# Kernel optimization log

Hardware: AMD Instinct MI355X
Metric: run time of the kernel (lower is better)

The kernel has to match this reference:

```python
import jax, jax.numpy as jnp
import numpy as np

K = 3
PAD = 1
STRIDE = 1


def _conv2d(x, w, b):
    out = jax.lax.conv_general_dilated(
        x, w, window_strides=(STRIDE, STRIDE),
        padding=[(PAD, PAD), (PAD, PAD)],
        dimension_numbers=("NCHW", "OIHW", "NCHW"))
    return out + b[None, :, None, None]


def setup_inputs() -> dict:
    key = jax.random.key(0)
    ks = jax.random.split(key, 6)
    B, C, H, W, O = 4, 64, 128, 128, 64
    x = jax.random.normal(ks[0], (B, C, H, W), dtype=jnp.float32)
    # small-scale offset/modulator weights so sampled offsets stay O(1) pixels
    offset_w = jax.random.normal(ks[1], (2 * K * K, C, K, K), dtype=jnp.float32) * 0.02
    offset_b = jax.random.normal(ks[2], (2 * K * K,), dtype=jnp.float32) * 0.02
    mod_w = jax.random.normal(ks[3], (K * K, C, K, K), dtype=jnp.float32) * 0.02
    mod_b = jax.random.normal(ks[4], (K * K,), dtype=jnp.float32) * 0.02
    weight = jax.random.normal(ks[5], (O, C, K, K), dtype=jnp.float32) * 0.05
    return {"x": x, "offset_w": offset_w, "offset_b": offset_b,
            "mod_w": mod_w, "mod_b": mod_b, "weight": weight}


def _deform_conv(x, offset, mask, weight):
    # torchvision deform_conv2d v2 semantics, zero padding outside the image.
    B, C, H, W = x.shape
    K2 = K * K
    Ho, Wo = offset.shape[2], offset.shape[3]
    dy = offset[:, 0::2]  # [B,K2,Ho,Wo] vertical offsets
    dx = offset[:, 1::2]  # [B,K2,Ho,Wo] horizontal offsets
    ky = jnp.repeat(jnp.arange(K), K).astype(x.dtype)   # kernel row per tap
    kx = jnp.tile(jnp.arange(K), K).astype(x.dtype)     # kernel col per tap
    oy = (jnp.arange(Ho) * STRIDE - PAD).astype(x.dtype)
    ox = (jnp.arange(Wo) * STRIDE - PAD).astype(x.dtype)
    py = oy[None, None, :, None] + ky[None, :, None, None] + dy  # [B,K2,Ho,Wo]
    px = ox[None, None, None, :] + kx[None, :, None, None] + dx

    y0 = jnp.floor(py)
    x0 = jnp.floor(px)
    wy1 = py - y0  # bilinear weights toward the +1 corner
    wx1 = px - x0
    y0i = y0.astype(jnp.int32)
    x0i = x0.astype(jnp.int32)

    xf = x.reshape(B, C, H * W)

    def gather(yc, xc, wgt):
        valid = ((yc >= 0) & (yc < H) & (xc >= 0) & (xc < W)).astype(x.dtype)
        idx = jnp.clip(yc, 0, H - 1) * W + jnp.clip(xc, 0, W - 1)  # [B,K2,Ho,Wo]
        flat = idx.reshape(B, 1, -1)
        g = jnp.take_along_axis(xf, jnp.broadcast_to(flat, (B, C, flat.shape[-1])), axis=2)
        g = g.reshape(B, C, K2, Ho, Wo)
        return g * (wgt * valid)[:, None]

    samp = (gather(y0i,     x0i,     (1 - wy1) * (1 - wx1))
            + gather(y0i,     x0i + 1, (1 - wy1) * wx1)
            + gather(y0i + 1, x0i,     wy1 * (1 - wx1))
            + gather(y0i + 1, x0i + 1, wy1 * wx1))  # [B,C,K2,Ho,Wo]

    wr = weight.reshape(weight.shape[0], C, K2)
    return jnp.einsum("ock,bckhw->bohw", wr, samp * mask[:, None])


def reference(x, offset_w, offset_b, mod_w, mod_b, weight):
    offset = _conv2d(x, offset_w, offset_b)
    mask = 2.0 * jax.nn.sigmoid(_conv2d(x, mod_w, mod_b))
    return _deform_conv(x, offset, mask, weight)
```

## Files before the change

kernel.cpp:

```cpp
#include <hip/hip_runtime.h>
#include <hip/hip_bf16.h>
#include <math.h>

typedef unsigned short u16;
typedef unsigned int   u32;
typedef __attribute__((ext_vector_type(8))) short short8;
typedef __attribute__((ext_vector_type(4))) float f32x4;

#define B_  4
#define C_  64
#define H_  128
#define W_  128
#define O_  64
#define HW_ (H_ * W_)

__device__ __forceinline__ u16 f2bf(float f) {
    __hip_bfloat16 h = __float2bfloat16(f);
    u16 u; __builtin_memcpy(&u, &h, 2); return u;
}
__device__ __forceinline__ float bf2f(u16 u) {
    return __uint_as_float((u32)u << 16);
}
__device__ __forceinline__ u32 pkbf(float lo, float hi) {
    return ((u32)f2bf(hi) << 16) | (u32)f2bf(lo);
}
__device__ __forceinline__ float bflo(u32 v) { return __uint_as_float(v << 16); }
__device__ __forceinline__ float bfhi(u32 v) { return __uint_as_float(v & 0xffff0000u); }

__device__ __forceinline__ uint4 interp8(
    uint4 c00, uint4 c01, uint4 c10, uint4 c11,
    float wtx, float wty, float wtz, float wtw)
{
    const u32* q00 = (const u32*)&c00;
    const u32* q01 = (const u32*)&c01;
    const u32* q10 = (const u32*)&c10;
    const u32* q11 = (const u32*)&c11;
    u32 bw[4];
#pragma unroll
    for (int q = 0; q < 4; ++q) {
        float slo = bflo(q00[q]) * wtx;
        slo = fmaf(bflo(q01[q]), wty, slo);
        slo = fmaf(bflo(q10[q]), wtz, slo);
        slo = fmaf(bflo(q11[q]), wtw, slo);
        float shi = bfhi(q00[q]) * wtx;
        shi = fmaf(bfhi(q01[q]), wty, shi);
        shi = fmaf(bfhi(q10[q]), wtz, shi);
        shi = fmaf(bfhi(q11[q]), wtw, shi);
        bw[q] = pkbf(slo, shi);
    }
    uint4 v; __builtin_memcpy(&v, bw, 16);
    return v;
}

__global__ __launch_bounds__(256) void prep(
    const float* __restrict__ x, const float* __restrict__ weight,
    const float* __restrict__ ow, const float* __restrict__ mw,
    u16* __restrict__ xt, u16* __restrict__ Wb, u16* __restrict__ OWb)
{
    int i = blockIdx.x, t = threadIdx.x;
    if (i < 1024) {
        __shared__ float tile[64][65];
        int lb = i >> 8;
        int pix0 = (i & 255) << 6;
        const float* xb = x + ((size_t)lb << 20);
#pragma unroll
        for (int it = 0; it < 16; ++it) {
            int e = it * 256 + t;
            int c = e >> 6, pl = e & 63;
            tile[c][pl] = xb[((size_t)c << 14) + pix0 + pl];
        }
        __syncthreads();
        u16* xo = xt + ((((size_t)lb << 14) + pix0) << 6);
#pragma unroll
        for (int it = 0; it < 4; ++it) {
            int e = it * 256 + t;
            int c4 = (e & 15) << 2;
            int pl = e >> 4;
            ushort4 v;
            v.x = f2bf(tile[c4 + 0][pl]);
            v.y = f2bf(tile[c4 + 1][pl]);
            v.z = f2bf(tile[c4 + 2][pl]);
            v.w = f2bf(tile[c4 + 3][pl]);
            *(ushort4*)&xo[((size_t)pl << 6) + c4] = v;
        }
    } else {
        int e = (i - 1024) * 256 + t;
        if (e < 36864) {
            int j = e & 7, ln = (e >> 3) & 63;
            int ks = (e >> 9) % 18, ot = e / 9216;
            int o = ot * 16 + (ln & 15);
            int kidx = ks * 32 + ((ln >> 4) << 3) + j;
            int k = kidx >> 6, c = kidx & 63;
            Wb[e] = f2bf(weight[((size_t)(o * 64 + c)) * 9 + k]);
        } else {
            int e2 = e - 36864;
            int j = e2 & 7, ln = (e2 >> 3) & 63;
            int ks = (e2 >> 9) % 18, ot = e2 / 9216;
            int o = ot * 16 + (ln & 15);
            int kidx = ks * 32 + ((ln >> 4) << 3) + j;
            int k = kidx >> 6, c = kidx & 63;
            float v = 0.0f;
            if (o < 18)      v = ow[((size_t)(o * 64 + c)) * 9 + k];
            else if (o < 27) v = mw[((size_t)((o - 18) * 64 + c)) * 9 + k];
            OWb[e2] = f2bf(v);
        }
    }
}

__global__ __launch_bounds__(256, 6) void fused_dcn(
    const u16* __restrict__ xt,
    const u16* __restrict__ Wb, const u16* __restrict__ OWb,
    const float* __restrict__ ob, const float* __restrict__ mb,
    float* __restrict__ out)
{
    __shared__ __align__(16) u16 S[16][576];
    __shared__ float   param[27][16];
    __shared__ __align__(16) int4    pwp[144];
    __shared__ __align__(16) ushort4 pww[144];

    const int t = threadIdx.x;
    const int lane = t & 63;
    const int wv = t >> 6;

    int bid0 = blockIdx.x;
    const int bid = (bid0 & 7) * 512 + (bid0 >> 3);
    const int lb = bid >> 10;
    const int pix0 = (bid & 1023) << 4;
    const int h  = pix0 >> 7;
    const int w0 = pix0 & 127;

    const u16* xtb = xt + ((size_t)lb << 20);
    const char* xb8 = (const char*)xtb;

#pragma unroll
    for (int i = 0; i < 4; ++i) {
        int e = i * 256 + t;
        int u = e >> 3, oct = e & 7;
        int k = u >> 4, pixl = u & 15;
        int ky = k / 3, kx = k - 3 * ky;
        int y = h - 1 + ky, xx = w0 + pixl - 1 + kx;
        bool valid = ((unsigned)y < 128u) && ((unsigned)xx < 128u);
        int idx = ((y & 127) << 7) + (xx & 127);
        uint4 v = *(const uint4*)(xtb + ((size_t)idx << 6) + (oct << 3));
        v.x = valid ? v.x : 0u;
        v.y = valid ? v.y : 0u;
        v.z = valid ? v.z : 0u;
        v.w = valid ? v.w : 0u;
        *(uint4*)&S[pixl][k * 64 + ((oct ^ (pixl & 7)) << 3)] = v;
    }
    if (t < 128) {
        int e = 1024 + t;
        int u = e >> 3, oct = e & 7;
        int pixl = u & 15;
        int y = h + 1;
        int xx = w0 + pixl - 1 + 2;
        bool valid = ((unsigned)y < 128u) && ((unsigned)xx < 128u);
        int idx = ((y & 127) << 7) + (xx & 127);
        uint4 v = *(const uint4*)(xtb + ((size_t)idx << 6) + (oct << 3));
        v.x = valid ? v.x : 0u;
        v.y = valid ? v.y : 0u;
        v.z = valid ? v.z : 0u;
        v.w = valid ? v.w : 0u;
        *(uint4*)&S[pixl][8 * 64 + ((oct ^ (pixl & 7)) << 3)] = v;
    }
    __syncthreads();

    if (wv < 2) {
        f32x4 k1 = {0.f, 0.f, 0.f, 0.f};
        int brow = lane & 15;
        int hi = lane >> 4;
        int swz = (brow & 7) << 3;
#pragma unroll
        for (int ks = 0; ks < 18; ++ks) {
            short8 a = ((const short8*)OWb)[(wv * 18 + ks) * 64 + lane];
            int coff = ((ks & 1) << 5) + (hi << 3);
            short8 bf = *(const short8*)&S[brow][(ks >> 1) * 64 + (coff ^ swz)];
            k1 = __builtin_amdgcn_mfma_f32_16x16x32_bf16(a, bf, k1, 0, 0, 0);
        }
#pragma unroll
        for (int r = 0; r < 4; ++r) {
            int oc = wv * 16 + (hi << 2) + r;
            if (oc < 18) {
                param[oc][brow] = k1[r] + ob[oc];
            } else if (oc < 27) {
                float s = k1[r] + mb[oc - 18];
                param[oc][brow] = 2.0f / (1.0f + __expf(-s));
            }
        }
    }
    __syncthreads();

    if (t < 144) {
        int tap = t >> 4, pixl = t & 15;
        int ky = tap / 3, kx = tap - 3 * ky;
        float dy = param[2 * tap][pixl];
        float dx = param[2 * tap + 1][pixl];
        float m  = param[18 + tap][pixl];
        float py = (float)(h - 1 + ky) + dy;
        float px = (float)(w0 + pixl - 1 + kx) + dx;
        float y0f = floorf(py), x0f = floorf(px);
        float fy = py - y0f, fx = px - x0f;
        int y0 = (int)y0f, x0 = (int)x0f;
        int y1 = y0 + 1, x1 = x0 + 1;
        bool vy0 = (unsigned)y0 < (unsigned)H_;
        bool vy1 = (unsigned)y1 < (unsigned)H_;
        bool vx0 = (unsigned)x0 < (unsigned)W_;
        bool vx1 = (unsigned)x1 < (unsigned)W_;
        float w00 = (1.f - fy) * (1.f - fx) * m; if (!(vy0 && vx0)) w00 = 0.f;
        float w01 = (1.f - fy) * fx          * m; if (!(vy0 && vx1)) w01 = 0.f;
        float w10 = fy * (1.f - fx)          * m; if (!(vy1 && vx0)) w10 = 0.f;
        float w11 = fy * fx                   * m; if (!(vy1 && vx1)) w11 = 0.f;
        int y0c = min(max(y0, 0), H_ - 1);
        int y1c = min(max(y1, 0), H_ - 1);
        int x0c = min(max(x0, 0), W_ - 1);
        int x1c = min(max(x1, 0), W_ - 1);
        pwp[t] = make_int4(((y0c << 7) + x0c) << 7, ((y0c << 7) + x1c) << 7,
                           ((y1c << 7) + x0c) << 7, ((y1c << 7) + x1c) << 7);
        pww[t] = make_ushort4(f2bf(w00), f2bf(w01), f2bf(w10), f2bf(w11));
    }
    __syncthreads();

    {
        const int oct = t & 7;
        const int ub  = t >> 3;
        int4 ofs0 = pwp[ub];       ushort4 wq0 = pww[ub];
        int4 ofs1 = pwp[ub + 32];  ushort4 wq1 = pww[ub + 32];
        int4 ofs2 = pwp[ub + 64];  ushort4 wq2 = pww[ub + 64];
        int4 ofs3 = pwp[ub + 96];  ushort4 wq3 = pww[ub + 96];
        const int co = oct << 4;
        uint4 a00 = *(const uint4*)(xb8 + ofs0.x + co);
        uint4 a01 = *(const uint4*)(xb8 + ofs0.y + co);
        uint4 a10 = *(const uint4*)(xb8 + ofs0.z + co);
        uint4 a11 = *(const uint4*)(xb8 + ofs0.w + co);
        uint4 b00 = *(const uint4*)(xb8 + ofs1.x + co);
        uint4 b01 = *(const uint4*)(xb8 + ofs1.y + co);
        uint4 b10 = *(const uint4*)(xb8 + ofs1.z + co);
        uint4 b11 = *(const uint4*)(xb8 + ofs1.w + co);
        uint4 c00 = *(const uint4*)(xb8 + ofs2.x + co);
        uint4 c01 = *(const uint4*)(xb8 + ofs2.y + co);
        uint4 c10 = *(const uint4*)(xb8 + ofs2.z + co);
        uint4 c11 = *(const uint4*)(xb8 + ofs2.w + co);
        uint4 d00 = *(const uint4*)(xb8 + ofs3.x + co);
        uint4 d01 = *(const uint4*)(xb8 + ofs3.y + co);
        uint4 d10 = *(const uint4*)(xb8 + ofs3.z + co);
        uint4 d11 = *(const uint4*)(xb8 + ofs3.w + co);
        __builtin_amdgcn_sched_barrier(0);
        {
            int k = ub >> 4, pixl = ub & 15;
            uint4 v = interp8(a00, a01, a10, a11,
                              bf2f(wq0.x), bf2f(wq0.y), bf2f(wq0.z), bf2f(wq0.w));
            *(uint4*)&S[pixl][k * 64 + ((oct ^ (pixl & 7)) << 3)] = v;
        }
        {
            int u1 = ub + 32;
            int k = u1 >> 4, pixl = u1 & 15;
            uint4 v = interp8(b00, b01, b10, b11,
                              bf2f(wq1.x), bf2f(wq1.y), bf2f(wq1.z), bf2f(wq1.w));
            *(uint4*)&S[pixl][k * 64 + ((oct ^ (pixl & 7)) << 3)] = v;
        }
        {
            int u2 = ub + 64;
            int k = u2 >> 4, pixl = u2 & 15;
            uint4 v = interp8(c00, c01, c10, c11,
                              bf2f(wq2.x), bf2f(wq2.y), bf2f(wq2.z), bf2f(wq2.w));
            *(uint4*)&S[pixl][k * 64 + ((oct ^ (pixl & 7)) << 3)] = v;
        }
        {
            int u3 = ub + 96;
            int k = u3 >> 4, pixl = u3 & 15;
            uint4 v = interp8(d00, d01, d10, d11,
                              bf2f(wq3.x), bf2f(wq3.y), bf2f(wq3.z), bf2f(wq3.w));
            *(uint4*)&S[pixl][k * 64 + ((oct ^ (pixl & 7)) << 3)] = v;
        }
    }
    if (t < 128) {
        int e = 1024 + t;
        int u = e >> 3, oct = e & 7;
        int pixl = u & 15;
        int4    ofs = pwp[u]; ushort4 wq = pww[u];
        uint4 c00 = *(const uint4*)(xb8 + ofs.x + (oct << 4));
        uint4 c01 = *(const uint4*)(xb8 + ofs.y + (oct << 4));
        uint4 c10 = *(const uint4*)(xb8 + ofs.z + (oct << 4));
        uint4 c11 = *(const uint4*)(xb8 + ofs.w + (oct << 4));
        uint4 v = interp8(c00, c01, c10, c11,
                          bf2f(wq.x), bf2f(wq.y), bf2f(wq.z), bf2f(wq.w));
        *(uint4*)&S[pixl][8 * 64 + ((oct ^ (pixl & 7)) << 3)] = v;
    }
    __syncthreads();

    {
        f32x4 acc = {0.f, 0.f, 0.f, 0.f};
        int brow = lane & 15;
        int hi = lane >> 4;
        int swz = (brow & 7) << 3;
#pragma unroll
        for (int ks = 0; ks < 18; ++ks) {
            int coff = ((ks & 1) << 5) + (hi << 3);
            short8 bfr = *(const short8*)&S[brow][(ks >> 1) * 64 + (coff ^ swz)];
            short8 a = ((const short8*)Wb)[(wv * 18 + ks) * 64 + lane];
            acc = __builtin_amdgcn_mfma_f32_16x16x32_bf16(a, bfr, acc, 0, 0, 0);
        }
        float* op = out + ((size_t)lb << 20) + pix0;
#pragma unroll
        for (int r = 0; r < 4; ++r) {
            int o = wv * 16 + (hi << 2) + r;
            op[((size_t)o << 14) + brow] = acc[r];
        }
    }
}

extern "C" void kernel_launch(void* const* d_in, const int* in_sizes, int n_in,
                              void* d_out, int out_size, void* d_ws, size_t ws_size,
                              hipStream_t stream)
{
    const float* x        = (const float*)d_in[0];
    const float* offset_w = (const float*)d_in[1];
    const float* offset_b = (const float*)d_in[2];
    const float* mod_w    = (const float*)d_in[3];
    const float* mod_b    = (const float*)d_in[4];
    const float* weight   = (const float*)d_in[5];
    float* out = (float*)d_out;

    u16* Wb  = (u16*)d_ws;
    u16* OWb = Wb + 36864;
    u16* xt  = OWb + 18432;

    prep<<<1240, 256, 0, stream>>>(x, weight, offset_w, mod_w, xt, Wb, OWb);
    fused_dcn<<<4096, 256, 0, stream>>>(xt, Wb, OWb, offset_b, mod_b, out);
}
```

Measured before the change: 44.16 us.

## Split offset conv across all waves with direct global loads and dual accumulators

The offset/modulator convolution previously staged the 3x3 neighborhood into shared memory and ran MFMAs on only two waves. Now all four waves compute it, each taking half of the K dimension and loading B fragments straight from global memory into registers. The two partial sums are reduced through shared memory that aliases the S buffer. This removes one staging pass and a barrier and balances the work across waves. Separately, the main GEMM uses two independent accumulators to break the MFMA dependency chain, and the prep transpose now reads float4 vectors.

```diff
diff --git a/kernel.cpp b/kernel.cpp
--- a/kernel.cpp
+++ b/kernel.cpp
@@ -64,10 +64,15 @@
         int pix0 = (i & 255) << 6;
         const float* xb = x + ((size_t)lb << 20);
 #pragma unroll
-        for (int it = 0; it < 16; ++it) {
+        for (int it = 0; it < 4; ++it) {
             int e = it * 256 + t;
-            int c = e >> 6, pl = e & 63;
-            tile[c][pl] = xb[((size_t)c << 14) + pix0 + pl];
+            int c = e >> 4;
+            int pl4 = (e & 15) << 2;
+            float4 v = *(const float4*)&xb[((size_t)c << 14) + pix0 + pl4];
+            tile[c][pl4 + 0] = v.x;
+            tile[c][pl4 + 1] = v.y;
+            tile[c][pl4 + 2] = v.z;
+            tile[c][pl4 + 3] = v.w;
         }
         __syncthreads();
         u16* xo = xt + ((((size_t)lb << 14) + pix0) << 6);
@@ -114,13 +119,16 @@
     float* __restrict__ out)
 {
     __shared__ __align__(16) u16 S[16][576];
-    __shared__ float   param[27][16];
     __shared__ __align__(16) int4    pwp[144];
-    __shared__ __align__(16) ushort4 pww[144];
+    __shared__ __align__(8)  ushort4 pww[144];
+
+    float* kpf = (float*)S;
 
     const int t = threadIdx.x;
     const int lane = t & 63;
     const int wv = t >> 6;
+    const int mypix = lane & 15;
+    const int hi = lane >> 4;
 
     int bid0 = blockIdx.x;
     const int bid = (bid0 & 7) * 512 + (bid0 >> 3);
@@ -132,72 +140,58 @@
     const u16* xtb = xt + ((size_t)lb << 20);
     const char* xb8 = (const char*)xtb;
 
-#pragma unroll
-    for (int i = 0; i < 4; ++i) {
-        int e = i * 256 + t;
-        int u = e >> 3, oct = e & 7;
-        int k = u >> 4, pixl = u & 15;
-        int ky = k / 3, kx = k - 3 * ky;
-        int y = h - 1 + ky, xx = w0 + pixl - 1 + kx;
-        bool valid = ((unsigned)y < 128u) && ((unsigned)xx < 128u);
-        int idx = ((y & 127) << 7) + (xx & 127);
-        uint4 v = *(const uint4*)(xtb + ((size_t)idx << 6) + (oct << 3));
-        v.x = valid ? v.x : 0u;
-        v.y = valid ? v.y : 0u;
-        v.z = valid ? v.z : 0u;
-        v.w = valid ? v.w : 0u;
-        *(uint4*)&S[pixl][k * 64 + ((oct ^ (pixl & 7)) << 3)] = v;
-    }
-    if (t < 128) {
-        int e = 1024 + t;
-        int u = e >> 3, oct = e & 7;
-        int pixl = u & 15;
-        int y = h + 1;
-        int xx = w0 + pixl - 1 + 2;
-        bool valid = ((unsigned)y < 128u) && ((unsigned)xx < 128u);
-        int idx = ((y & 127) << 7) + (xx & 127);
-        uint4 v = *(const uint4*)(xtb + ((size_t)idx << 6) + (oct << 3));
-        v.x = valid ? v.x : 0u;
-        v.y = valid ? v.y : 0u;
-        v.z = valid ? v.z : 0u;
-        v.w = valid ? v.w : 0u;
-        *(uint4*)&S[pixl][8 * 64 + ((oct ^ (pixl & 7)) << 3)] = v;
+    {
+        const int ot = wv & 1, kh = wv >> 1;
+        f32x4 k1 = {0.f, 0.f, 0.f, 0.f};
+        uint4 raw[9];
+#pragma unroll
+        for (int q = 0; q < 9; ++q) {
+            int ks = kh * 9 + q;
+            int tap = ks >> 1;
+            int ky = tap / 3, kx = tap - 3 * ky;
+            int y  = h - 1 + ky;
+            int xx = w0 + mypix - 1 + kx;
+            int idx = ((y & 127) << 7) + (xx & 127);
+            raw[q] = *(const uint4*)(xtb + ((size_t)idx << 6) + ((ks & 1) << 5) + (hi << 3));
+        }
+        __builtin_amdgcn_sched_barrier(0);
+#pragma unroll
+        for (int q = 0; q < 9; ++q) {
+            int ks = kh * 9 + q;
+            int tap = ks >> 1;
+            int ky = tap / 3, kx = tap - 3 * ky;
+            int y  = h - 1 + ky;
+            int xx = w0 + mypix - 1 + kx;
+            bool valid = ((unsigned)y < 128u) && ((unsigned)xx < 128u);
+            uint4 rw = raw[q];
+            rw.x = valid ? rw.x : 0u;
+            rw.y = valid ? rw.y : 0u;
+            rw.z = valid ? rw.z : 0u;
+            rw.w = valid ? rw.w : 0u;
+            short8 bfr;
+            __builtin_memcpy(&bfr, &rw, 16);
+            short8 wa = ((const short8*)OWb)[(ot * 18 + ks) * 64 + lane];
+            k1 = __builtin_amdgcn_mfma_f32_16x16x32_bf16(wa, bfr, k1, 0, 0, 0);
+        }
+#pragma unroll
+        for (int r = 0; r < 4; ++r)
+            kpf[((kh << 1) + ot) * 256 + ((hi << 2) + r) * 16 + mypix] = k1[r];
     }
     __syncthreads();
 
-    if (wv < 2) {
-        f32x4 k1 = {0.f, 0.f, 0.f, 0.f};
-        int brow = lane & 15;
-        int hi = lane >> 4;
-        int swz = (brow & 7) << 3;
-#pragma unroll
-        for (int ks = 0; ks < 18; ++ks) {
-            short8 a = ((const short8*)OWb)[(wv * 18 + ks) * 64 + lane];
-            int coff = ((ks & 1) << 5) + (hi << 3);
-            short8 bf = *(const short8*)&S[brow][(ks >> 1) * 64 + (coff ^ swz)];
-            k1 = __builtin_amdgcn_mfma_f32_16x16x32_bf16(a, bf, k1, 0, 0, 0);
-        }
-#pragma unroll
-        for (int r = 0; r < 4; ++r) {
-            int oc = wv * 16 + (hi << 2) + r;
-            if (oc < 18) {
-                param[oc][brow] = k1[r] + ob[oc];
-            } else if (oc < 27) {
-                float s = k1[r] + mb[oc - 18];
-                param[oc][brow] = 2.0f / (1.0f + __expf(-s));
-            }
-        }
-    }
-    __syncthreads();
-
     if (t < 144) {
-        int tap = t >> 4, pixl = t & 15;
+        int tap = t >> 4, pix = t & 15;
         int ky = tap / 3, kx = tap - 3 * ky;
-        float dy = param[2 * tap][pixl];
-        float dx = param[2 * tap + 1][pixl];
-        float m  = param[18 + tap][pixl];
+        int ocy = 2 * tap, ocx = 2 * tap + 1, ocm = 18 + tap;
+        float dy = kpf[((ocy >> 4)) * 256 + (ocy & 15) * 16 + pix]
+                 + kpf[512 + ((ocy >> 4)) * 256 + (ocy & 15) * 16 + pix] + ob[ocy];
+        float dx = kpf[((ocx >> 4)) * 256 + (ocx & 15) * 16 + pix]
+                 + kpf[512 + ((ocx >> 4)) * 256 + (ocx & 15) * 16 + pix] + ob[ocx];
+        float sm = kpf[256 + (ocm - 16) * 16 + pix]
+                 + kpf[512 + 256 + (ocm - 16) * 16 + pix] + mb[tap];
+        float m  = 2.0f / (1.0f + __expf(-sm));
         float py = (float)(h - 1 + ky) + dy;
-        float px = (float)(w0 + pixl - 1 + kx) + dx;
+        float px = (float)(w0 + pix - 1 + kx) + dx;
         float y0f = floorf(py), x0f = floorf(px);
         float fy = py - y0f, fx = px - x0f;
         int y0 = (int)y0f, x0 = (int)x0f;
@@ -289,22 +283,26 @@
     __syncthreads();
 
     {
-        f32x4 acc = {0.f, 0.f, 0.f, 0.f};
+        f32x4 acca = {0.f, 0.f, 0.f, 0.f};
+        f32x4 accb = {0.f, 0.f, 0.f, 0.f};
         int brow = lane & 15;
-        int hi = lane >> 4;
+        int hi2 = lane >> 4;
         int swz = (brow & 7) << 3;
 #pragma unroll
-        for (int ks = 0; ks < 18; ++ks) {
-            int coff = ((ks & 1) << 5) + (hi << 3);
-            short8 bfr = *(const short8*)&S[brow][(ks >> 1) * 64 + (coff ^ swz)];
-            short8 a = ((const short8*)Wb)[(wv * 18 + ks) * 64 + lane];
-            acc = __builtin_amdgcn_mfma_f32_16x16x32_bf16(a, bfr, acc, 0, 0, 0);
+        for (int kp = 0; kp < 9; ++kp) {
+            int ks0 = kp * 2, ks1 = kp * 2 + 1;
+            short8 b0 = *(const short8*)&S[brow][kp * 64 + ((hi2 << 3) ^ swz)];
+            short8 b1 = *(const short8*)&S[brow][kp * 64 + ((32 + (hi2 << 3)) ^ swz)];
+            short8 a0 = ((const short8*)Wb)[(wv * 18 + ks0) * 64 + lane];
+            short8 a1 = ((const short8*)Wb)[(wv * 18 + ks1) * 64 + lane];
+            acca = __builtin_amdgcn_mfma_f32_16x16x32_bf16(a0, b0, acca, 0, 0, 0);
+            accb = __builtin_amdgcn_mfma_f32_16x16x32_bf16(a1, b1, accb, 0, 0, 0);
         }
         float* op = out + ((size_t)lb << 20) + pix0;
 #pragma unroll
         for (int r = 0; r < 4; ++r) {
-            int o = wv * 16 + (hi << 2) + r;
-            op[((size_t)o << 14) + brow] = acc[r];
+            int o = wv * 16 + (hi2 << 2) + r;
+            op[((size_t)o << 14) + brow] = acca[r] + accb[r];
         }
     }
 }
```

Result: slower. 56.55 us (+28.1%).
